# Optimization experiments

Hardware: AMD Instinct MI355X
Metric: run time of the kernel (lower is better)

## Reference

```python
import jax, jax.numpy as jnp
import numpy as np

B, S, D = 2, 2048, 1024
H, HD = 16, 64          # num_heads, head_dim (D == H*HD)
FF = 4 * D
EPS = 1e-5

def _xavier(key, shape):
    fan_out, fan_in = shape
    lim = np.sqrt(6.0 / (fan_in + fan_out))
    return jax.random.uniform(key, shape, jnp.float32, -lim, lim)

def setup_inputs() -> dict:
    key = jax.random.key(0)
    ks = jax.random.split(key, 8)
    return {
        "x": jax.random.normal(ks[0], (B, S, D), jnp.float32),
        "g1": jnp.ones((D,), jnp.float32), "b1": jnp.zeros((D,), jnp.float32),
        "Wqkv": _xavier(ks[1], (3 * D, D)), "bqkv": jnp.zeros((3 * D,), jnp.float32),
        "Wo": _xavier(ks[2], (D, D)), "bo": jnp.zeros((D,), jnp.float32),
        "g2": jnp.ones((D,), jnp.float32), "b2": jnp.zeros((D,), jnp.float32),
        "W1": _xavier(ks[3], (FF, D)), "b1m": jnp.zeros((FF,), jnp.float32),
        "W2": _xavier(ks[4], (D, FF)), "b2m": jnp.zeros((D,), jnp.float32),
    }

def _ln(x, g, b):
    m = jnp.mean(x, axis=-1, keepdims=True)
    v = jnp.var(x, axis=-1, keepdims=True)
    return (x - m) * jax.lax.rsqrt(v + EPS) * g + b

def reference(x, g1, b1, Wqkv, bqkv, Wo, bo, g2, b2, W1, b1m, W2, b2m):
    # --- pre-norm attention ---
    h = _ln(x, g1, b1)
    qkv = h @ Wqkv.T + bqkv                                  # [B,S,3D]
    qkv = qkv.reshape(B, S, H, 3 * HD).transpose(0, 2, 1, 3)  # [B,H,S,3hd]
    q, k, v = jnp.split(qkv, 3, axis=-1)                      # each [B,H,S,hd]
    scores = jnp.einsum('bhqd,bhkd->bhqk', q, k) / np.sqrt(HD).astype(np.float32)
    att = jax.nn.softmax(scores, axis=-1)                     # [B,H,S,S]
    vals = jnp.einsum('bhqk,bhkd->bhqd', att, v)
    vals = vals.transpose(0, 2, 1, 3).reshape(B, S, D)
    x = x + (vals @ Wo.T + bo)
    # --- pre-norm MLP (dropouts inactive in eval) ---
    h = _ln(x, g2, b2)
    h = jax.nn.gelu(h @ W1.T + b1m, approximate=False)
    x = x + (h @ W2.T + b2m)
    return x
```

## Files before the change

### kernel.cpp

```cpp
#include <hip/hip_runtime.h>
#include <math.h>

#define BB 2
#define SS 2048
#define DD 1024
#define HH 16
#define FFDIM 4096
#define NROWS 4096

typedef short bf16x8 __attribute__((ext_vector_type(8)));
typedef float f32x4 __attribute__((ext_vector_type(4)));

__device__ __forceinline__ unsigned short f2bf(float f) {
    unsigned u = __float_as_uint(f);
    u += 0x7fffu + ((u >> 16) & 1u);
    return (unsigned short)(u >> 16);
}
__device__ __forceinline__ float bf2f(unsigned short s) {
    return __uint_as_float(((unsigned)s) << 16);
}

typedef __attribute__((address_space(1))) void gvoid;
typedef __attribute__((address_space(3))) void lvoid;
__device__ __forceinline__ void glds16(const void* g, void* l) {
    __builtin_amdgcn_global_load_lds((gvoid*)g, (lvoid*)l, 16, 0, 0);
}

__device__ __forceinline__ int vkey(int kloc) {
    return (kloc & ~31) + ((kloc & 12) << 1) + ((kloc & 16) >> 2);
}

__device__ __forceinline__ void ln_body(const float* __restrict__ x,
                                        const float* __restrict__ g,
                                        const float* __restrict__ b,
                                        unsigned short* __restrict__ out, int row) {
    const float* xr = x + (size_t)row * DD;
    unsigned short* orow = out + (size_t)row * DD;
    int t = threadIdx.x;
    float4 v = ((const float4*)xr)[t];
    float s  = v.x + v.y + v.z + v.w;
    float s2 = v.x*v.x + v.y*v.y + v.z*v.z + v.w*v.w;
    #pragma unroll
    for (int off = 32; off > 0; off >>= 1) {
        s  += __shfl_down(s,  off);
        s2 += __shfl_down(s2, off);
    }
    __shared__ float red1[4], red2[4];
    int wid = t >> 6, lane = t & 63;
    if (lane == 0) { red1[wid] = s; red2[wid] = s2; }
    __syncthreads();
    if (t == 0) {
        float a = 0.f, a2 = 0.f;
        #pragma unroll
        for (int i = 0; i < 4; ++i) { a += red1[i]; a2 += red2[i]; }
        red1[0] = a; red2[0] = a2;
    }
    __syncthreads();
    float mean = red1[0] * (1.0f / DD);
    float var  = red2[0] * (1.0f / DD) - mean * mean;
    float rs = rsqrtf(var + 1e-5f);
    float4 gv = ((const float4*)g)[t];
    float4 bv = ((const float4*)b)[t];
    ushort4 o;
    o.x = f2bf((v.x - mean) * rs * gv.x + bv.x);
    o.y = f2bf((v.y - mean) * rs * gv.y + bv.y);
    o.z = f2bf((v.z - mean) * rs * gv.z + bv.z);
    o.w = f2bf((v.w - mean) * rs * gv.w + bv.w);
    ((ushort4*)orow)[t] = o;
}

__global__ __launch_bounds__(256) void ln_kernel(const float* __restrict__ x,
                                                 const float* __restrict__ g,
                                                 const float* __restrict__ b,
                                                 unsigned short* __restrict__ out) {
    ln_body(x, g, b, out, blockIdx.x);
}

__global__ __launch_bounds__(256) void prep_kernel(
    const float* __restrict__ x, const float* __restrict__ g1,
    const float* __restrict__ b1, unsigned short* __restrict__ hb,
    const float* __restrict__ a, unsigned short* __restrict__ oa,
    const float* __restrict__ b, unsigned short* __restrict__ ob,
    const float* __restrict__ c, unsigned short* __restrict__ oc,
    const float* __restrict__ d, unsigned short* __restrict__ od) {
    if (blockIdx.x < 4096) { ln_body(x, g1, b1, hb, blockIdx.x); return; }
    int i = (blockIdx.x - 4096) * 256 + threadIdx.x;
    const float* src; unsigned short* dst; int off;
    if (i < 786432)       { src = a; dst = oa; off = i; }
    else if (i < 1048576) { src = b; dst = ob; off = i - 786432; }
    else if (i < 2097152) { src = c; dst = oc; off = i - 1048576; }
    else                  { src = d; dst = od; off = i - 2097152; }
    float4 v = ((const float4*)src)[off];
    ushort4 o;
    o.x = f2bf(v.x); o.y = f2bf(v.y); o.z = f2bf(v.z); o.w = f2bf(v.w);
    ((ushort4*)dst)[off] = o;
}

__global__ __launch_bounds__(256) void reduce_add(const float* __restrict__ x1,
                                                  const unsigned short* __restrict__ P0,
                                                  const unsigned short* __restrict__ P1,
                                                  const float* __restrict__ bias,
                                                  float* __restrict__ out) {
    int i = blockIdx.x * 256 + threadIdx.x;
    float4 a = ((const float4*)x1)[i];
    ushort4 p = ((const ushort4*)P0)[i];
    ushort4 q = ((const ushort4*)P1)[i];
    float4 bv = ((const float4*)bias)[i & 255];
    float4 o;
    o.x = a.x + bf2f(p.x) + bf2f(q.x) + bv.x;
    o.y = a.y + bf2f(p.y) + bf2f(q.y) + bv.y;
    o.z = a.z + bf2f(p.z) + bf2f(q.z) + bv.z;
    o.w = a.w + bf2f(p.w) + bf2f(q.w) + bv.w;
    ((float4*)out)[i] = o;
}

template<int ACT, int RES, int OUTBF, int TN, int VT, int CS, int SPLITK, int SWZ>
__global__ __launch_bounds__(256, 3) void gemm_nt_mfma(
    const unsigned short* __restrict__ A,
    const unsigned short* __restrict__ W,
    const float* __restrict__ bias,
    const float* __restrict__ res,
    void* __restrict__ Cout,
    void* __restrict__ Cout2,
    unsigned short* __restrict__ Vtg,
    int M, int N, int K)
{
    constexpr int MI = (TN == 128) ? 4 : 2;
    constexpr int WR = TN / 4;
    __shared__ unsigned short SMEM[128 * 64 + TN * 64];
    unsigned short* As = SMEM;
    unsigned short* Ws = SMEM + 128 * 64;
    int tid = threadIdx.x;
    int lane = tid & 63;
    int w = tid >> 6;
    int rowbase = (TN == 128) ? ((w >> 1) * 64) : (w * 32);
    int colbase = (TN == 128) ? ((w & 1) * 64) : 0;
    int col16 = lane & 15, quad = lane >> 4;

    int bx, by, bz;
    if constexpr (SWZ) {
        int nx = gridDim.x, nz = gridDim.z;
        int bid = blockIdx.x + nx * (blockIdx.y + 32 * blockIdx.z);
        int xcd = bid & 7;
        int g = bid >> 3;
        int per = nx * nz;
        by = xcd + 8 * (g / per);
        int r = g % per;
        bx = r % nx;
        bz = r / nx;
    } else { bx = blockIdx.x; by = blockIdx.y; bz = blockIdx.z; }
    int bm = by * 128, bn = bx * TN;

    int klen = SPLITK ? (K >> 1) : K;
    int kbase = SPLITK ? (bz * klen) : 0;

    f32x4 acc[MI][4] = {};

    int lrow = lane >> 3;
    int sw = (lane & 7) ^ lrow;
    const unsigned short* Ag = A + (size_t)(bm + w * 32 + lrow) * K + sw * 8;
    const unsigned short* Wg = W + (size_t)(bn + w * WR + lrow) * K + sw * 8;

    for (int k0 = kbase; k0 < kbase + klen; k0 += 64) {
        if (k0 != kbase) __syncthreads();
        #pragma unroll
        for (int it = 0; it < 4; ++it)
            glds16(Ag + (size_t)(8 * it) * K + k0, &As[(w * 32 + 8 * it) * 64]);
        #pragma unroll
        for (int it = 0; it < WR / 8; ++it)
            glds16(Wg + (size_t)(8 * it) * K + k0, &Ws[(w * WR + 8 * it) * 64]);
        __syncthreads();
        #pragma unroll
        for (int c = 0; c < 2; ++c) {
            bf16x8 af[MI], bfr[4];
            #pragma unroll
            for (int i = 0; i < MI; ++i) {
                int m = rowbase + i * 16 + col16;
                af[i] = *(const bf16x8*)&As[m * 64 + (((c * 4 + quad) ^ (m & 7)) * 8)];
            }
            #pragma unroll
            for (int j = 0; j < 4; ++j) {
                int n = colbase + j * 16 + col16;
                bfr[j] = *(const bf16x8*)&Ws[n * 64 + (((c * 4 + quad) ^ (n & 7)) * 8)];
            }
            #pragma unroll
            for (int i = 0; i < MI; ++i)
                #pragma unroll
                for (int j = 0; j < 4; ++j)
                    acc[i][j] = __builtin_amdgcn_mfma_f32_16x16x32_bf16(af[i], bfr[j], acc[i][j], 0, 0, 0);
        }
    }

    if constexpr (SPLITK) {
        unsigned short* P = (unsigned short*)(bz ? Cout2 : Cout);
        #pragma unroll
        for (int i = 0; i < MI; ++i) {
            #pragma unroll
            for (int j = 0; j < 4; ++j) {
                int nn = bn + colbase + j * 16 + col16;
                #pragma unroll
                for (int r = 0; r < 4; ++r) {
                    int mm = bm + rowbase + i * 16 + quad * 4 + r;
                    P[(size_t)mm * N + nn] = f2bf(acc[i][j][r]);
                }
            }
        }
        return;
    }

    if constexpr (CS) {
        __syncthreads();
        #pragma unroll
        for (int i = 0; i < MI; ++i) {
            #pragma unroll
            for (int j = 0; j < 4; ++j) {
                int nl = colbase + j * 16 + col16;
                float bv = bias[bn + nl];
                int c = nl >> 4;
                #pragma unroll
                for (int r = 0; r < 4; ++r) {
                    int ml = rowbase + i * 16 + quad * 4 + r;
                    float v = acc[i][j][r] + bv;
                    if (ACT) {
                        float z = v * (1.595769122f + 0.071354816f * v * v);
                        float e = __builtin_amdgcn_exp2f(-z * 1.442695041f);
                        v = v * __builtin_amdgcn_rcpf(1.0f + e);
                    }
                    SMEM[ml * 128 + ((c ^ ((ml >> 2) & 7)) << 4) + (nl & 15)] = f2bf(v);
                }
            }
        }
        __syncthreads();
        #pragma unroll
        for (int p = 0; p < 8; ++p) {
            int cid = tid + p * 256;
            int row = cid >> 4, cc = cid & 15;
            int cs2 = cc >> 1;
            bf16x8 vv = *(bf16x8*)&SMEM[row * 128 + ((cs2 ^ ((row >> 2) & 7)) << 4) + (cc & 1) * 8];
            *(bf16x8*)&((unsigned short*)Cout)[(size_t)(bm + row) * N + bn + cc * 8] = vv;
        }
        return;
    }

    bool wave_v = VT && ((((bn + colbase) >> 6) % 3) == 2);
    if constexpr (VT) __syncthreads();

    #pragma unroll
    for (int i = 0; i < MI; ++i) {
        #pragma unroll
        for (int j = 0; j < 4; ++j) {
            int nn = bn + colbase + j * 16 + col16;
            float bv = bias[nn];
            float vv[4];
            #pragma unroll
            for (int r = 0; r < 4; ++r) {
                float v = acc[i][j][r] + bv;
                if (ACT) {
                    float z = v * (1.595769122f + 0.071354816f * v * v);
                    float e = __builtin_amdgcn_exp2f(-z * 1.442695041f);
                    v = v * __builtin_amdgcn_rcpf(1.0f + e);
                }
                vv[r] = v;
            }
            int mm0 = bm + rowbase + i * 16 + quad * 4;
            if (VT && wave_v) {
                int d = j * 16 + col16;
                int kloc = rowbase + i * 16 + quad * 4;
                int vl = vkey(kloc);
                int ch = vl >> 3;
                ushort4 pk;
                pk.x = f2bf(vv[0]); pk.y = f2bf(vv[1]);
                pk.z = f2bf(vv[2]); pk.w = f2bf(vv[3]);
                *(ushort4*)&SMEM[d * 128 + ((ch ^ (d & 7)) << 3) + (vl & 7)] = pk;
            } else {
                #pragma unroll
                for (int r = 0; r < 4; ++r) {
                    int mm = mm0 + r;
                    float v = vv[r];
                    if (RES) v += res[(size_t)mm * N + nn];
                    if (OUTBF) ((unsigned short*)Cout)[(size_t)mm * N + nn] = f2bf(v);
                    else       ((float*)Cout)[(size_t)mm * N + nn] = v;
                }
            }
        }
    }

    if constexpr (VT) {
        __syncthreads();
        bool g0v = ((bn >> 6) % 3) == 2;
        bool g1v = (((bn + 64) >> 6) % 3) == 2;
        if (g0v || g1v) {
            int vcb = g0v ? 0 : 64;
            int hh = (bn + vcb) / 192;
            int bb = bm >> 11, sr = bm & 2047;
            #pragma unroll
            for (int p = 0; p < 4; ++p) {
                int cid = tid + p * 256;
                int d = cid >> 4, ch = cid & 15;
                bf16x8 vv2 = *(bf16x8*)&SMEM[d * 128 + ((ch ^ (d & 7)) << 3)];
                *(bf16x8*)&Vtg[((size_t)((bb * HH + hh) * 64 + d)) * (size_t)SS + sr + ch * 8] = vv2;
            }
        }
    }
}

__global__ __launch_bounds__(256, 3) void attn_mfma(
    const unsigned short* __restrict__ qkv,
    const unsigned short* __restrict__ Vtg,
    unsigned short* __restrict__ outb)
{
    __shared__ unsigned short Ks[128 * 64];
    __shared__ unsigned short VtL[64 * 128];
    int tid = threadIdx.x;
    int lane = tid & 63;
    int wv = tid >> 6;
    int qt = blockIdx.x, h = blockIdx.y, b = blockIdx.z;
    int col16 = lane & 15, quad = lane >> 4;

    const unsigned short* qbase = qkv + (size_t)(b * SS) * 3072;
    const unsigned short* Kg = qbase + h * 192 + 64;
    const unsigned short* Vg = Vtg + ((size_t)(b * HH + h) * 64) * (size_t)SS;

    const float C = 0.18033688011112042f;
    bf16x8 qf[2][2];
    #pragma unroll
    for (int qq = 0; qq < 2; ++qq) {
        int qrow = qt * 128 + qq * 64 + wv * 16 + col16;
        qf[qq][0] = *(const bf16x8*)&qbase[(size_t)qrow * 3072 + h * 192 + quad * 8];
        qf[qq][1] = *(const bf16x8*)&qbase[(size_t)qrow * 3072 + h * 192 + 32 + quad * 8];
        #pragma unroll
        for (int c = 0; c < 2; ++c)
            #pragma unroll
            for (int i = 0; i < 8; ++i) {
                float f = __uint_as_float(((unsigned)(unsigned short)qf[qq][c][i]) << 16) * C;
                qf[qq][c][i] = (short)f2bf(f);
            }
    }

    f32x4 o[2][4] = {};
    float lsum[2] = {0.f, 0.f};

    for (int s0 = 0; s0 < SS; s0 += 128) {
        if (s0) __syncthreads();
        #pragma unroll
        for (int p = 0; p < 4; ++p) {
            int ci = (p * 4 + wv) * 64 + lane;
            int k = ci >> 3, sk = ci & 7, qk = sk ^ (k & 7);
            glds16(Kg + (size_t)(s0 + k) * 3072 + qk * 8, &Ks[ci * 8]);
            int dv = ci >> 4, sv = ci & 15, qv = sv ^ (dv & 7);
            glds16(Vg + (size_t)dv * SS + s0 + qv * 8, &VtL[ci * 8]);
        }
        __syncthreads();

        #pragma unroll
        for (int qq = 0; qq < 2; ++qq) {
            f32x4 st[8];
            #pragma unroll
            for (int t = 0; t < 8; ++t) {
                f32x4 z = {};
                st[t] = z;
                int key = t * 16 + col16;
                #pragma unroll
                for (int c = 0; c < 2; ++c) {
                    bf16x8 kf = *(const bf16x8*)&Ks[key * 64 + (((c * 4 + quad) ^ (key & 7)) * 8)];
                    st[t] = __builtin_amdgcn_mfma_f32_16x16x32_bf16(kf, qf[qq][c], st[t], 0, 0, 0);
                }
            }

            unsigned lo[8], hi[8];
            float psum = 0.f;
            #pragma unroll
            for (int t = 0; t < 8; ++t) {
                float p0 = __builtin_amdgcn_exp2f(st[t][0]);
                float p1 = __builtin_amdgcn_exp2f(st[t][1]);
                float p2 = __builtin_amdgcn_exp2f(st[t][2]);
                float p3 = __builtin_amdgcn_exp2f(st[t][3]);
                psum += (p0 + p1) + (p2 + p3);
                lo[t] = __builtin_amdgcn_perm(__float_as_uint(p1), __float_as_uint(p0), 0x07060302u);
                hi[t] = __builtin_amdgcn_perm(__float_as_uint(p3), __float_as_uint(p2), 0x07060302u);
            }
            psum += __shfl_xor(psum, 16);
            psum += __shfl_xor(psum, 32);
            lsum[qq] += psum;

            #pragma unroll
            for (int kc = 0; kc < 4; ++kc) {
                uint4 pk;
                pk.x = lo[2 * kc]; pk.y = hi[2 * kc];
                pk.z = lo[2 * kc + 1]; pk.w = hi[2 * kc + 1];
                bf16x8 pf = *(bf16x8*)&pk;
                #pragma unroll
                for (int nt = 0; nt < 4; ++nt) {
                    int d = nt * 16 + col16;
                    bf16x8 vf = *(const bf16x8*)&VtL[d * 128 + (((kc * 4 + quad) ^ (d & 7)) * 8)];
                    o[qq][nt] = __builtin_amdgcn_mfma_f32_16x16x32_bf16(pf, vf, o[qq][nt], 0, 0, 0);
                }
            }
        }
    }

    #pragma unroll
    for (int qq = 0; qq < 2; ++qq) {
        float linv = __builtin_amdgcn_rcpf(lsum[qq]);
        float linv_r[4];
        #pragma unroll
        for (int r = 0; r < 4; ++r) linv_r[r] = __shfl(linv, quad * 4 + r);
        int orow0 = b * SS + qt * 128 + qq * 64 + wv * 16;
        #pragma unroll
        for (int r = 0; r < 4; ++r) {
            int mm = orow0 + quad * 4 + r;
            #pragma unroll
            for (int nt = 0; nt < 4; ++nt)
                outb[(size_t)mm * DD + h * 64 + nt * 16 + col16] = f2bf(o[qq][nt][r] * linv_r[r]);
        }
    }
}

extern "C" void kernel_launch(void* const* d_in, const int* in_sizes, int n_in,
                              void* d_out, int out_size, void* d_ws, size_t ws_size,
                              hipStream_t stream) {
    const float* x    = (const float*)d_in[0];
    const float* g1   = (const float*)d_in[1];
    const float* b1   = (const float*)d_in[2];
    const float* Wqkv = (const float*)d_in[3];
    const float* bqkv = (const float*)d_in[4];
    const float* Wo   = (const float*)d_in[5];
    const float* bo   = (const float*)d_in[6];
    const float* g2   = (const float*)d_in[7];
    const float* b2   = (const float*)d_in[8];
    const float* W1   = (const float*)d_in[9];
    const float* b1m  = (const float*)d_in[10];
    const float* W2   = (const float*)d_in[11];
    const float* b2m  = (const float*)d_in[12];
    float* out = (float*)d_out;

    char* wsb = (char*)d_ws;
    unsigned short* Wq_b  = (unsigned short*)(wsb);
    unsigned short* Wo_b  = (unsigned short*)(wsb + 6291456);
    unsigned short* W1_b  = (unsigned short*)(wsb + 8388608);
    unsigned short* W2_b  = (unsigned short*)(wsb + 16777216);
    unsigned short* hb    = (unsigned short*)(wsb + 25165824);
    unsigned short* qkvb  = (unsigned short*)(wsb + 33554432);
    unsigned short* attnb = (unsigned short*)(wsb + 58720256);
    float*          x1    = (float*)(wsb + 67108864);
    unsigned short* ffb   = (unsigned short*)(wsb + 83886080);
    unsigned short* Vtg   = (unsigned short*)(wsb + 83886080);
    unsigned short* P0    = (unsigned short*)(wsb + 33554432);
    unsigned short* P1    = (unsigned short*)(wsb + 41943040);

    prep_kernel<<<16384, 256, 0, stream>>>(x, g1, b1, hb,
                                           Wqkv, Wq_b, Wo, Wo_b, W1, W1_b, W2, W2_b);
    gemm_nt_mfma<0,0,1,128,1,0,0,1><<<dim3(24, 32), 256, 0, stream>>>(hb, Wq_b, bqkv, nullptr, qkvb,
                                                                      nullptr, Vtg, NROWS, 3 * DD, DD);
    attn_mfma<<<dim3(SS / 128, HH, BB), 256, 0, stream>>>(qkvb, Vtg, attnb);
    gemm_nt_mfma<0,1,0,64,0,0,0,1><<<dim3(16, 32), 256, 0, stream>>>(attnb, Wo_b, bo, x, x1,
                                                                     nullptr, nullptr, NROWS, DD, DD);
    ln_kernel<<<NROWS, 256, 0, stream>>>(x1, g2, b2, hb);
    gemm_nt_mfma<1,0,1,128,0,1,0,1><<<dim3(32, 32), 256, 0, stream>>>(hb, W1_b, b1m, nullptr, ffb,
                                                                      nullptr, nullptr, NROWS, FFDIM, DD);
    gemm_nt_mfma<0,0,0,128,0,0,1,1><<<dim3(8, 32, 2), 256, 0, stream>>>(ffb, W2_b, nullptr, nullptr, P0,
                                                                        P1, nullptr, NROWS, DD, FFDIM);
    reduce_add<<<4096, 256, 0, stream>>>(x1, P0, P1, b2m, out);
}
```

Measured before the change: 313.8 us.

## Halve attention query tile to 64 rows and double block count

After: 317.7 us. Within noise of the previous version (+1.2%).

```diff
diff --git a/kernel.cpp b/kernel.cpp
--- a/kernel.cpp
+++ b/kernel.cpp
@@ -304,7 +304,7 @@
     }
 }
 
-__global__ __launch_bounds__(256, 3) void attn_mfma(
+__global__ __launch_bounds__(256, 4) void attn_mfma(
     const unsigned short* __restrict__ qkv,
     const unsigned short* __restrict__ Vtg,
     unsigned short* __restrict__ outb)
@@ -322,23 +322,20 @@
     const unsigned short* Vg = Vtg + ((size_t)(b * HH + h) * 64) * (size_t)SS;
 
     const float C = 0.18033688011112042f;
-    bf16x8 qf[2][2];
+    int qrow = qt * 64 + wv * 16 + col16;
+    bf16x8 qf[2];
+    qf[0] = *(const bf16x8*)&qbase[(size_t)qrow * 3072 + h * 192 + quad * 8];
+    qf[1] = *(const bf16x8*)&qbase[(size_t)qrow * 3072 + h * 192 + 32 + quad * 8];
     #pragma unroll
-    for (int qq = 0; qq < 2; ++qq) {
-        int qrow = qt * 128 + qq * 64 + wv * 16 + col16;
-        qf[qq][0] = *(const bf16x8*)&qbase[(size_t)qrow * 3072 + h * 192 + quad * 8];
-        qf[qq][1] = *(const bf16x8*)&qbase[(size_t)qrow * 3072 + h * 192 + 32 + quad * 8];
-        #pragma unroll
-        for (int c = 0; c < 2; ++c)
-            #pragma unroll
-            for (int i = 0; i < 8; ++i) {
-                float f = __uint_as_float(((unsigned)(unsigned short)qf[qq][c][i]) << 16) * C;
-                qf[qq][c][i] = (short)f2bf(f);
-            }
-    }
-
-    f32x4 o[2][4] = {};
-    float lsum[2] = {0.f, 0.f};
+    for (int c = 0; c < 2; ++c)
+        #pragma unroll
+        for (int i = 0; i < 8; ++i) {
+            float f = __uint_as_float(((unsigned)(unsigned short)qf[c][i]) << 16) * C;
+            qf[c][i] = (short)f2bf(f);
+        }
+
+    f32x4 o[4] = {};
+    float lsum = 0.f;
 
     for (int s0 = 0; s0 < SS; s0 += 128) {
         if (s0) __syncthreads();
@@ -352,67 +349,62 @@
         }
         __syncthreads();
 
-        #pragma unroll
-        for (int qq = 0; qq < 2; ++qq) {
-            f32x4 st[8];
-            #pragma unroll
-            for (int t = 0; t < 8; ++t) {
-                f32x4 z = {};
-                st[t] = z;
-                int key = t * 16 + col16;
-                #pragma unroll
-                for (int c = 0; c < 2; ++c) {
-                    bf16x8 kf = *(const bf16x8*)&Ks[key * 64 + (((c * 4 + quad) ^ (key & 7)) * 8)];
-                    st[t] = __builtin_amdgcn_mfma_f32_16x16x32_bf16(kf, qf[qq][c], st[t], 0, 0, 0);
-                }
-            }
-
-            unsigned lo[8], hi[8];
-            float psum = 0.f;
-            #pragma unroll
-            for (int t = 0; t < 8; ++t) {
-                float p0 = __builtin_amdgcn_exp2f(st[t][0]);
-                float p1 = __builtin_amdgcn_exp2f(st[t][1]);
-                float p2 = __builtin_amdgcn_exp2f(st[t][2]);
-                float p3 = __builtin_amdgcn_exp2f(st[t][3]);
-                psum += (p0 + p1) + (p2 + p3);
-                lo[t] = __builtin_amdgcn_perm(__float_as_uint(p1), __float_as_uint(p0), 0x07060302u);
-                hi[t] = __builtin_amdgcn_perm(__float_as_uint(p3), __float_as_uint(p2), 0x07060302u);
-            }
-            psum += __shfl_xor(psum, 16);
-            psum += __shfl_xor(psum, 32);
-            lsum[qq] += psum;
-
-            #pragma unroll
-            for (int kc = 0; kc < 4; ++kc) {
-                uint4 pk;
-                pk.x = lo[2 * kc]; pk.y = hi[2 * kc];
-                pk.z = lo[2 * kc + 1]; pk.w = hi[2 * kc + 1];
-                bf16x8 pf = *(bf16x8*)&pk;
-                #pragma unroll
-                for (int nt = 0; nt < 4; ++nt) {
-                    int d = nt * 16 + col16;
-                    bf16x8 vf = *(const bf16x8*)&VtL[d * 128 + (((kc * 4 + quad) ^ (d & 7)) * 8)];
-                    o[qq][nt] = __builtin_amdgcn_mfma_f32_16x16x32_bf16(pf, vf, o[qq][nt], 0, 0, 0);
-                }
-            }
-        }
-    }
-
+        f32x4 st[8];
+        #pragma unroll
+        for (int t = 0; t < 8; ++t) {
+            f32x4 z = {};
+            st[t] = z;
+            int key = t * 16 + col16;
+            #pragma unroll
+            for (int c = 0; c < 2; ++c) {
+                bf16x8 kf = *(const bf16x8*)&Ks[key * 64 + (((c * 4 + quad) ^ (key & 7)) * 8)];
+                st[t] = __builtin_amdgcn_mfma_f32_16x16x32_bf16(kf, qf[c], st[t], 0, 0, 0);
+            }
+        }
+
+        unsigned lo[8], hi[8];
+        float psum = 0.f;
+        #pragma unroll
+        for (int t = 0; t < 8; ++t) {
+            float p0 = __builtin_amdgcn_exp2f(st[t][0]);
+            float p1 = __builtin_amdgcn_exp2f(st[t][1]);
+            float p2 = __builtin_amdgcn_exp2f(st[t][2]);
+            float p3 = __builtin_amdgcn_exp2f(st[t][3]);
+            psum += (p0 + p1) + (p2 + p3);
+            lo[t] = __builtin_amdgcn_perm(__float_as_uint(p1), __float_as_uint(p0), 0x07060302u);
+            hi[t] = __builtin_amdgcn_perm(__float_as_uint(p3), __float_as_uint(p2), 0x07060302u);
+        }
+        psum += __shfl_xor(psum, 16);
+        psum += __shfl_xor(psum, 32);
+        lsum += psum;
+
+        #pragma unroll
+        for (int kc = 0; kc < 4; ++kc) {
+            uint4 pk;
+            pk.x = lo[2 * kc]; pk.y = hi[2 * kc];
+            pk.z = lo[2 * kc + 1]; pk.w = hi[2 * kc + 1];
+            bf16x8 pf = *(bf16x8*)&pk;
+            #pragma unroll
+            for (int nt = 0; nt < 4; ++nt) {
+                int d = nt * 16 + col16;
+                bf16x8 vf = *(const bf16x8*)&VtL[d * 128 + (((kc * 4 + quad) ^ (d & 7)) * 8)];
+                o[nt] = __builtin_amdgcn_mfma_f32_16x16x32_bf16(pf, vf, o[nt], 0, 0, 0);
+            }
+        }
+    }
+
+    float linv = __builtin_amdgcn_rcpf(lsum);
+    float linv_r[4];
     #pragma unroll
-    for (int qq = 0; qq < 2; ++qq) {
-        float linv = __builtin_amdgcn_rcpf(lsum[qq]);
-        float linv_r[4];
-        #pragma unroll
-        for (int r = 0; r < 4; ++r) linv_r[r] = __shfl(linv, quad * 4 + r);
-        int orow0 = b * SS + qt * 128 + qq * 64 + wv * 16;
-        #pragma unroll
-        for (int r = 0; r < 4; ++r) {
-            int mm = orow0 + quad * 4 + r;
-            #pragma unroll
-            for (int nt = 0; nt < 4; ++nt)
-                outb[(size_t)mm * DD + h * 64 + nt * 16 + col16] = f2bf(o[qq][nt][r] * linv_r[r]);
-        }
+    for (int r = 0; r < 4; ++r) linv_r[r] = __shfl(linv, quad * 4 + r);
+
+    int orow0 = b * SS + qt * 64 + wv * 16;
+    #pragma unroll
+    for (int r = 0; r < 4; ++r) {
+        int mm = orow0 + quad * 4 + r;
+        #pragma unroll
+        for (int nt = 0; nt < 4; ++nt)
+            outb[(size_t)mm * DD + h * 64 + nt * 16 + col16] = f2bf(o[nt][r] * linv_r[r]);
     }
 }
 
@@ -452,7 +444,7 @@
                                            Wqkv, Wq_b, Wo, Wo_b, W1, W1_b, W2, W2_b);
     gemm_nt_mfma<0,0,1,128,1,0,0,1><<<dim3(24, 32), 256, 0, stream>>>(hb, Wq_b, bqkv, nullptr, qkvb,
                                                                       nullptr, Vtg, NROWS, 3 * DD, DD);
-    attn_mfma<<<dim3(SS / 128, HH, BB), 256, 0, stream>>>(qkvb, Vtg, attnb);
+    attn_mfma<<<dim3(SS / 64, HH, BB), 256, 0, stream>>>(qkvb, Vtg, attnb);
     gemm_nt_mfma<0,1,0,64,0,0,0,1><<<dim3(16, 32), 256, 0, stream>>>(attnb, Wo_b, bo, x, x1,
                                                                      nullptr, nullptr, NROWS, DD, DD);
     ln_kernel<<<NROWS, 256, 0, stream>>>(x1, g2, b2, hb);
```
